# Optimization experiments

Measured on AMD Instinct MI355X. Metric: run time of the kernel, lower is better.

Reference implementation:

```python
import jax, jax.numpy as jnp
import numpy as np

N = 50000
E = 1600000
F_IN = 3
C = 40

def _linear_params(key, fan_in, fan_out):
    k1, k2 = jax.random.split(key)
    bound = 1.0 / np.sqrt(fan_in)
    W = jax.random.uniform(k1, (fan_in, fan_out), jnp.float32, -bound, bound)
    b = jax.random.uniform(k2, (fan_out,), jnp.float32, -bound, bound)
    return W, b

def setup_inputs() -> dict:
    key = jax.random.key(0)
    ks = jax.random.split(key, 9)
    x = jax.random.normal(ks[0], (N, F_IN), jnp.float32)
    pos = jax.random.normal(ks[1], (N, 3), jnp.float32)
    edge_index = jax.random.randint(ks[2], (2, E), 0, N, jnp.int64)
    W1, b1 = _linear_params(ks[3], F_IN + 3, 64)   # local_nn layer 1
    W2, b2 = _linear_params(ks[4], 64, 64)          # local_nn layer 2
    W3, b3 = _linear_params(ks[5], 64, 128)         # global_nn layer 1
    W4, b4 = _linear_params(ks[6], 128, 1024)       # global_nn layer 2
    W5, b5 = _linear_params(ks[7], 1024, 64)        # global_nn layer 3
    Wf, bf = _linear_params(ks[8], 64, C)           # fc
    return {"x": x, "pos": pos, "edge_index": edge_index,
            "W1": W1, "b1": b1, "W2": W2, "b2": b2,
            "W3": W3, "b3": b3, "W4": W4, "b4": b4,
            "W5": W5, "b5": b5, "Wf": Wf, "bf": bf}

def reference(x, pos, edge_index, W1, b1, W2, b2, W3, b3, W4, b4, W5, b5, Wf, bf):
    # PyG PointNetConv: add self-loops by default
    loop = jnp.arange(N, dtype=edge_index.dtype)
    src = jnp.concatenate([edge_index[0], loop])  # j
    dst = jnp.concatenate([edge_index[1], loop])  # i
    # message: local_nn(concat(x_j, pos_j - pos_i))  -> [E+N, 64]
    msg_in = jnp.concatenate([x[src], pos[src] - pos[dst]], axis=1)
    h = jax.nn.relu(msg_in @ W1 + b1)
    h = h @ W2 + b2
    # max-aggregate to destination nodes
    agg = jax.ops.segment_max(h, dst, num_segments=N)
    # global_nn
    g = jax.nn.relu(agg @ W3 + b3)
    g = jax.nn.relu(g @ W4 + b4)
    g = g @ W5 + b5
    # trailing relu + fc + log_softmax
    out = jax.nn.relu(g) @ Wf + bf
    return jax.nn.log_softmax(out, axis=1)
```

## Files before the change

### kernel.cpp

```cpp
#include <hip/hip_runtime.h>
#include <cstddef>
#include <cmath>

typedef __attribute__((ext_vector_type(8))) short bf16x8;
typedef __attribute__((ext_vector_type(4))) float f32x4;

static __device__ __forceinline__ f32x4 mfma16(bf16x8 a, bf16x8 b, f32x4 c) {
    return __builtin_amdgcn_mfma_f32_16x16x32_bf16(a, b, c, 0, 0, 0);
}
static __device__ __forceinline__ unsigned short f2bf(float f) {
    unsigned int u = __float_as_uint(f);
    return (unsigned short)((u + 0x7FFFu + ((u >> 16) & 1u)) >> 16);
}

#define NBK 256

__global__ __launch_bounds__(256) void k_hist(const int* __restrict__ ei, int E,
                                              unsigned int* __restrict__ ghist) {
    __shared__ unsigned int h[NBK];
    int tid = threadIdx.x;
    h[tid] = 0u;
    __syncthreads();
    int idx = blockIdx.x * 256 + tid;
    int e0 = idx * 4;
    if (e0 + 3 < E) {
        int4 d = ((const int4*)(ei + E))[idx];
        atomicAdd(&h[d.x >> 8], 1u);
        atomicAdd(&h[d.y >> 8], 1u);
        atomicAdd(&h[d.z >> 8], 1u);
        atomicAdd(&h[d.w >> 8], 1u);
    } else {
        for (int e = e0; e < E; ++e) atomicAdd(&h[ei[E + e] >> 8], 1u);
    }
    __syncthreads();
    unsigned int c = h[tid];
    if (c) atomicAdd(&ghist[tid], c);
}

__global__ __launch_bounds__(256) void k_bscan(const unsigned int* __restrict__ ghist,
                                               unsigned int* __restrict__ bbase,
                                               unsigned int* __restrict__ gcur) {
    __shared__ unsigned int s[NBK];
    int t = threadIdx.x;
    unsigned int c = ghist[t];
    s[t] = c;
    __syncthreads();
    for (int d = 1; d < 256; d <<= 1) {
        unsigned int v = (t >= d) ? s[t - d] : 0u;
        __syncthreads();
        s[t] += v;
        __syncthreads();
    }
    bbase[t] = s[t] - c;
    gcur[t] = 0u;
}

__global__ __launch_bounds__(256) void k_bin(const int* __restrict__ ei, int E,
                                             const unsigned int* __restrict__ bbase,
                                             unsigned int* __restrict__ gcur,
                                             unsigned int* __restrict__ pairs) {
    __shared__ unsigned int h[NBK];
    __shared__ unsigned int base[NBK];
    int tid = threadIdx.x;
    h[tid] = 0u;
    __syncthreads();
    int idx = blockIdx.x * 256 + tid;
    int e0 = idx * 4;
    unsigned int vals[4]; int bs[4]; unsigned int rk[4]; int cnt4 = 0;
    if (e0 + 3 < E) {
        int4 s = ((const int4*)ei)[idx];
        int4 d = ((const int4*)(ei + E))[idx];
        int sa[4] = {s.x, s.y, s.z, s.w};
        int da[4] = {d.x, d.y, d.z, d.w};
        cnt4 = 4;
#pragma unroll
        for (int j = 0; j < 4; ++j) {
            bs[j] = da[j] >> 8;
            vals[j] = (unsigned int)sa[j] | ((unsigned int)(da[j] & 255) << 16);
            rk[j] = atomicAdd(&h[bs[j]], 1u);
        }
    } else {
        for (int e = e0; e < E; ++e) {
            int j = cnt4++;
            int sv = ei[e], dv = ei[E + e];
            bs[j] = dv >> 8;
            vals[j] = (unsigned int)sv | ((unsigned int)(dv & 255) << 16);
            rk[j] = atomicAdd(&h[bs[j]], 1u);
        }
    }
    __syncthreads();
    unsigned int c = h[tid];
    base[tid] = c ? atomicAdd(&gcur[tid], c) : 0u;
    __syncthreads();
    for (int j = 0; j < cnt4; ++j)
        pairs[bbase[bs[j]] + base[bs[j]] + rk[j]] = vals[j];
}

__global__ __launch_bounds__(256) void k_build(const unsigned int* __restrict__ ghist,
                                               const unsigned int* __restrict__ bbase,
                                               const unsigned int* __restrict__ pairs,
                                               unsigned int* __restrict__ list,
                                               unsigned int* __restrict__ off,
                                               unsigned int* __restrict__ deg, int N) {
    __shared__ unsigned int cntL[NBK];
    __shared__ unsigned int s[NBK];
    __shared__ unsigned int curL[NBK];
    int b = blockIdx.x, t = threadIdx.x;
    unsigned int gstart = bbase[b];
    unsigned int m = ghist[b];
    cntL[t] = 0u;
    __syncthreads();
    for (unsigned int i = t; i < m; i += 256u)
        atomicAdd(&cntL[(pairs[gstart + i] >> 16) & 255u], 1u);
    __syncthreads();
    unsigned int c = cntL[t];
    s[t] = c;
    __syncthreads();
    for (int d = 1; d < 256; d <<= 1) {
        unsigned int v = (t >= d) ? s[t - d] : 0u;
        __syncthreads();
        s[t] += v;
        __syncthreads();
    }
    unsigned int excl = s[t] - c;
    int dst = b * 256 + t;
    if (dst < N) { off[dst] = gstart + excl; deg[dst] = c; }
    curL[t] = excl;
    __syncthreads();
    for (unsigned int i = t; i < m; i += 256u) {
        unsigned int v = pairs[gstart + i];
        unsigned int p = atomicAdd(&curL[(v >> 16) & 255u], 1u);
        list[gstart + p] = v & 0xFFFFu;
    }
}

__global__ void k_convert(const float* __restrict__ W1, const float* __restrict__ W2,
                          const float* __restrict__ W3, const float* __restrict__ W4,
                          const float* __restrict__ W5,
                          unsigned short* __restrict__ W1bt, unsigned short* __restrict__ W2bt,
                          unsigned short* __restrict__ W3bt, unsigned short* __restrict__ W4bt,
                          unsigned short* __restrict__ W5ct) {
    int id = blockIdx.x * 256 + threadIdx.x;
    if (id < 2048) {
        int n = id >> 5, k = id & 31;
        W1bt[id] = (k < 6) ? f2bf(W1[k * 64 + n]) : (unsigned short)0;
    } else if (id < 2048 + 4096) {
        int t = id - 2048;
        int n = t >> 6, k = t & 63;
        W2bt[t] = f2bf(W2[k * 64 + n]);
    } else if (id < 6144 + 8192) {
        int t = id - 6144;
        int n = t >> 6, k = t & 63;
        W3bt[t] = f2bf(W3[k * 128 + n]);
    } else if (id < 14336 + 131072) {
        int t = id - 14336;
        int n = t >> 7, k = t & 127;
        W4bt[t] = f2bf(W4[k * 1024 + n]);
    } else if (id < 145408 + 65536) {
        int t = id - 145408;
        int ch = t >> 11, rem = t & 2047;
        int n = rem >> 5, kl = rem & 31;
        W5ct[t] = f2bf(W5[(ch * 32 + kl) * 64 + n]);
    }
}

#define TPB_E 256
#define EDGE_WPB 4
__global__ __launch_bounds__(TPB_E, 3) void edge_kernel(
    const float* __restrict__ x, const float* __restrict__ pos,
    const unsigned int* __restrict__ off, const unsigned int* __restrict__ deg,
    const unsigned int* __restrict__ list,
    const unsigned short* __restrict__ W1bt, const float* __restrict__ b1,
    const unsigned short* __restrict__ W2bt, const float* __restrict__ b2,
    float* __restrict__ agg, int N, int dstStride)
{
    __shared__ __align__(16) short Hs[4][16 * 72];

    int tid = threadIdx.x;
    int lane = tid & 63;
    int w = tid >> 6;
    int lm = lane & 15;
    int quad = lane >> 4;
    short* H = Hs[w];
    int dst0 = blockIdx.x * EDGE_WPB + w;

    bf16x8 B1f[4], B2f[4][2];
    float b1c[4], b2c[4];
#pragma unroll
    for (int nt = 0; nt < 4; ++nt) {
        B1f[nt] = *(const bf16x8*)&W1bt[(nt * 16 + lm) * 32 + quad * 8];
        B2f[nt][0] = *(const bf16x8*)&W2bt[(nt * 16 + lm) * 64 + quad * 8];
        B2f[nt][1] = *(const bf16x8*)&W2bt[(nt * 16 + lm) * 64 + 32 + quad * 8];
        b1c[nt] = b1[nt * 16 + lm];
        b2c[nt] = b2[nt * 16 + lm];
    }

    for (int dst = dst0; dst < N; dst += dstStride) {
        unsigned int o0 = off[dst];
        int ecnt = (int)deg[dst];
        int M = ecnt + 1;
        float pi0 = pos[dst * 3 + 0], pi1 = pos[dst * 3 + 1], pi2 = pos[dst * 3 + 2];

        float m0 = -INFINITY, m1 = -INFINITY, m2 = -INFINITY, m3 = -INFINITY;

        for (int base = 0; base < M; base += 16) {
            bf16x8 A = {0, 0, 0, 0, 0, 0, 0, 0};
            if (quad == 0) {
                int i = min(base + lm, M - 1);
                int s = (i == 0) ? dst : (int)list[o0 + i - 1];
                A[0] = (short)f2bf(x[s * 3 + 0]);
                A[1] = (short)f2bf(x[s * 3 + 1]);
                A[2] = (short)f2bf(x[s * 3 + 2]);
                A[3] = (short)f2bf(pos[s * 3 + 0] - pi0);
                A[4] = (short)f2bf(pos[s * 3 + 1] - pi1);
                A[5] = (short)f2bf(pos[s * 3 + 2] - pi2);
            }
#pragma unroll
            for (int nt = 0; nt < 4; ++nt) {
                f32x4 c = {0.f, 0.f, 0.f, 0.f};
                c = mfma16(A, B1f[nt], c);
#pragma unroll
                for (int r = 0; r < 4; ++r) {
                    float v = fmaxf(c[r] + b1c[nt], 0.f);
                    H[(quad * 4 + r) * 72 + nt * 16 + lm] = (short)f2bf(v);
                }
            }
            bf16x8 A2a = *(const bf16x8*)&H[lm * 72 + quad * 8];
            bf16x8 A2b = *(const bf16x8*)&H[lm * 72 + 32 + quad * 8];
            {
                f32x4 c = {0.f, 0.f, 0.f, 0.f};
                c = mfma16(A2a, B2f[0][0], c); c = mfma16(A2b, B2f[0][1], c);
                m0 = fmaxf(m0, fmaxf(fmaxf(c[0], c[1]), fmaxf(c[2], c[3])));
            }
            {
                f32x4 c = {0.f, 0.f, 0.f, 0.f};
                c = mfma16(A2a, B2f[1][0], c); c = mfma16(A2b, B2f[1][1], c);
                m1 = fmaxf(m1, fmaxf(fmaxf(c[0], c[1]), fmaxf(c[2], c[3])));
            }
            {
                f32x4 c = {0.f, 0.f, 0.f, 0.f};
                c = mfma16(A2a, B2f[2][0], c); c = mfma16(A2b, B2f[2][1], c);
                m2 = fmaxf(m2, fmaxf(fmaxf(c[0], c[1]), fmaxf(c[2], c[3])));
            }
            {
                f32x4 c = {0.f, 0.f, 0.f, 0.f};
                c = mfma16(A2a, B2f[3][0], c); c = mfma16(A2b, B2f[3][1], c);
                m3 = fmaxf(m3, fmaxf(fmaxf(c[0], c[1]), fmaxf(c[2], c[3])));
            }
        }

        m0 = fmaxf(m0, __shfl_xor(m0, 16, 64)); m0 = fmaxf(m0, __shfl_xor(m0, 32, 64));
        m1 = fmaxf(m1, __shfl_xor(m1, 16, 64)); m1 = fmaxf(m1, __shfl_xor(m1, 32, 64));
        m2 = fmaxf(m2, __shfl_xor(m2, 16, 64)); m2 = fmaxf(m2, __shfl_xor(m2, 32, 64));
        m3 = fmaxf(m3, __shfl_xor(m3, 16, 64)); m3 = fmaxf(m3, __shfl_xor(m3, 32, 64));

        float mv = (quad == 0) ? m0 : (quad == 1) ? m1 : (quad == 2) ? m2 : m3;
        agg[(size_t)dst * 64 + lane] = mv + b2c[quad];
    }
}

#define NNODE 64
__global__ __launch_bounds__(256, 3) void node_kernel(
    const float* __restrict__ agg,
    const unsigned short* __restrict__ W3bt, const float* __restrict__ b3,
    const unsigned short* __restrict__ W4bt, const float* __restrict__ b4,
    const unsigned short* __restrict__ W5ct, const float* __restrict__ b5,
    const float* __restrict__ Wf, const float* __restrict__ bf,
    float* __restrict__ out, int N)
{
    __shared__ __align__(16) char smem[50176];
    short* G1t = (short*)smem;
    float* G3f = (float*)smem;
    short* G2t = (short*)(smem + 17408);
    short* Wb4 = (short*)(smem + 22528);
    short* Wb5 = (short*)(smem + 39936);
    float* os  = (float*)(smem + 17408);

    int tid = threadIdx.x;
    int lane = tid & 63;
    int wm = tid >> 6;
    int lm = lane & 15;
    int quad = lane >> 4;
    int n0 = blockIdx.x * NNODE;

    auto stage = [&](int ch, int buf) {
        const unsigned short* g4 = W4bt + (size_t)ch * 4096;
        short* d4 = Wb4 + buf * 4352;
#pragma unroll
        for (int it = 0; it < 2; ++it) {
            int v = tid + it * 256;
            *(int4*)&d4[(v >> 4) * 136 + (v & 15) * 8] = *(const int4*)(g4 + v * 8);
        }
        const unsigned short* g5 = W5ct + (size_t)ch * 2048;
        short* d5 = Wb5 + buf * 2560;
        {
            int v = tid;
            *(int4*)&d5[(v >> 2) * 40 + (v & 3) * 8] = *(const int4*)(g5 + v * 8);
        }
    };

    stage(0, 0);

    {
        int arow = min(n0 + wm * 16 + lm, N - 1);
        bf16x8 A3[2];
#pragma unroll
        for (int f = 0; f < 2; ++f) {
            const float* p = agg + (size_t)arow * 64 + f * 32 + quad * 8;
            float4 u = *(const float4*)p;
            float4 v = *(const float4*)(p + 4);
            bf16x8 t;
            t[0] = (short)f2bf(u.x); t[1] = (short)f2bf(u.y);
            t[2] = (short)f2bf(u.z); t[3] = (short)f2bf(u.w);
            t[4] = (short)f2bf(v.x); t[5] = (short)f2bf(v.y);
            t[6] = (short)f2bf(v.z); t[7] = (short)f2bf(v.w);
            A3[f] = t;
        }
#pragma unroll
        for (int nt = 0; nt < 8; ++nt) {
            const unsigned short* wb = W3bt + (nt * 16 + lm) * 64 + quad * 8;
            f32x4 c = {0.f, 0.f, 0.f, 0.f};
            c = mfma16(*(const bf16x8*)wb, A3[0], c);
            c = mfma16(*(const bf16x8*)(wb + 32), A3[1], c);
            float4 bb = *(const float4*)&b3[nt * 16 + quad * 4];
            unsigned int u0 = (unsigned int)f2bf(fmaxf(c[0] + bb.x, 0.f)) |
                              ((unsigned int)f2bf(fmaxf(c[1] + bb.y, 0.f)) << 16);
            unsigned int u1 = (unsigned int)f2bf(fmaxf(c[2] + bb.z, 0.f)) |
                              ((unsigned int)f2bf(fmaxf(c[3] + bb.w, 0.f)) << 16);
            *(uint2*)&G1t[(wm * 16 + lm) * 136 + nt * 16 + quad * 4] = make_uint2(u0, u1);
        }
    }

    bf16x8 A4[4];
#pragma unroll
    for (int f = 0; f < 4; ++f)
        A4[f] = *(const bf16x8*)&G1t[(wm * 16 + lm) * 136 + f * 32 + quad * 8];

    f32x4 acc3[4];
#pragma unroll
    for (int nt = 0; nt < 4; ++nt) {
        float b = b5[nt * 16 + lm];
        acc3[nt][0] = b; acc3[nt][1] = b; acc3[nt][2] = b; acc3[nt][3] = b;
    }

    __syncthreads();

    for (int ch = 0; ch < 32; ++ch) {
        int buf = ch & 1;
        if (ch < 31) stage(ch + 1, buf ^ 1);

        const short* w4b = Wb4 + buf * 4352;
        const short* w5b = Wb5 + buf * 2560;

#pragma unroll
        for (int t = 0; t < 2; ++t) {
            f32x4 c = {0.f, 0.f, 0.f, 0.f};
#pragma unroll
            for (int kc = 0; kc < 4; ++kc)
                c = mfma16(*(const bf16x8*)&w4b[(t * 16 + lm) * 136 + kc * 32 + quad * 8],
                           A4[kc], c);
            float4 bb = *(const float4*)&b4[ch * 32 + t * 16 + quad * 4];
            unsigned int u0 = (unsigned int)f2bf(fmaxf(c[0] + bb.x, 0.f)) |
                              ((unsigned int)f2bf(fmaxf(c[1] + bb.y, 0.f)) << 16);
            unsigned int u1 = (unsigned int)f2bf(fmaxf(c[2] + bb.z, 0.f)) |
                              ((unsigned int)f2bf(fmaxf(c[3] + bb.w, 0.f)) << 16);
            *(uint2*)&G2t[(wm * 16 + lm) * 40 + t * 16 + quad * 4] = make_uint2(u0, u1);
        }
        bf16x8 A5 = *(const bf16x8*)&G2t[(wm * 16 + lm) * 40 + quad * 8];
#pragma unroll
        for (int nt = 0; nt < 4; ++nt)
            acc3[nt] = mfma16(A5, *(const bf16x8*)&w5b[(nt * 16 + lm) * 40 + quad * 8],
                              acc3[nt]);
        __syncthreads();
    }

#pragma unroll
    for (int nt = 0; nt < 4; ++nt)
#pragma unroll
        for (int r = 0; r < 4; ++r)
            G3f[(wm * 16 + quad * 4 + r) * 68 + nt * 16 + lm] = fmaxf(acc3[nt][r], 0.f);
    __syncthreads();

    for (int idx = tid; idx < NNODE * 40; idx += 256) {
        int ln = idx / 40;
        int c = idx - ln * 40;
        float o = bf[c];
#pragma unroll 4
        for (int j = 0; j < 64; ++j)
            o = fmaf(G3f[ln * 68 + j], Wf[j * 40 + c], o);
        os[ln * 41 + c] = o;
    }
    __syncthreads();

    if (tid < NNODE && n0 + tid < N) {
        int ln = tid;
        float mx = os[ln * 41 + 0];
#pragma unroll
        for (int c = 1; c < 40; ++c) mx = fmaxf(mx, os[ln * 41 + c]);
        float s = 0.f;
#pragma unroll
        for (int c = 0; c < 40; ++c) s += expf(os[ln * 41 + c] - mx);
        float ls = logf(s) + mx;
        float* op = out + (size_t)(n0 + tid) * 40;
#pragma unroll
        for (int c = 0; c < 40; ++c) op[c] = os[ln * 41 + c] - ls;
    }
}

extern "C" void kernel_launch(void* const* d_in, const int* in_sizes, int n_in,
                              void* d_out, int out_size, void* d_ws, size_t ws_size,
                              hipStream_t stream) {
    const float* x   = (const float*)d_in[0];
    const float* pos = (const float*)d_in[1];
    const int*   ei  = (const int*)d_in[2];
    const float* W1  = (const float*)d_in[3];
    const float* b1  = (const float*)d_in[4];
    const float* W2  = (const float*)d_in[5];
    const float* b2  = (const float*)d_in[6];
    const float* W3  = (const float*)d_in[7];
    const float* b3  = (const float*)d_in[8];
    const float* W4  = (const float*)d_in[9];
    const float* b4  = (const float*)d_in[10];
    const float* W5  = (const float*)d_in[11];
    const float* b5  = (const float*)d_in[12];
    const float* Wf  = (const float*)d_in[13];
    const float* bf  = (const float*)d_in[14];
    float* out = (float*)d_out;

    int Nn = in_sizes[0] / 3;
    int E  = in_sizes[2] / 2;

    char* w = (char*)d_ws;
    size_t p = 0;
    auto take = [&](size_t bytes) { size_t q = p; p = (p + bytes + 255) & ~size_t(255); return (void*)(w + q); };
    unsigned int*   off   = (unsigned int*)take((size_t)Nn * 4);
    unsigned int*   deg   = (unsigned int*)take((size_t)Nn * 4);
    unsigned int*   ghist = (unsigned int*)take(NBK * 4);
    unsigned int*   bbase = (unsigned int*)take(NBK * 4);
    unsigned int*   gcur  = (unsigned int*)take(NBK * 4);
    unsigned int*   list  = (unsigned int*)take((size_t)E * 4);
    float*          agg   = (float*)take((size_t)Nn * 64 * 4);
    unsigned int*   pairs = (unsigned int*)agg;
    unsigned short* W1bt = (unsigned short*)take(2048 * 2);
    unsigned short* W2bt = (unsigned short*)take(4096 * 2);
    unsigned short* W3bt = (unsigned short*)take(8192 * 2);
    unsigned short* W4bt = (unsigned short*)take(131072 * 2);
    unsigned short* W5ct = (unsigned short*)take(65536 * 2);

    k_convert<<<(2048 + 4096 + 8192 + 131072 + 65536 + 255) / 256, 256, 0, stream>>>(
        W1, W2, W3, W4, W5, W1bt, W2bt, W3bt, W4bt, W5ct);

    hipMemsetAsync(ghist, 0, NBK * 4, stream);
    int q4 = (E + 3) / 4;
    int gb = (q4 + 255) / 256;
    k_hist<<<gb, 256, 0, stream>>>(ei, E, ghist);
    k_bscan<<<1, 256, 0, stream>>>(ghist, bbase, gcur);
    k_bin<<<gb, 256, 0, stream>>>(ei, E, bbase, gcur, pairs);
    int nb = (Nn + 255) >> 8;
    k_build<<<nb, 256, 0, stream>>>(ghist, bbase, pairs, list, off, deg, Nn);

    int totalWaves = (Nn + 3) / 4;
    int eBlocks = (totalWaves + EDGE_WPB - 1) / EDGE_WPB;
    int dstStride = eBlocks * EDGE_WPB;
    edge_kernel<<<eBlocks, TPB_E, 0, stream>>>(
        x, pos, off, deg, list, W1bt, b1, W2bt, b2, agg, Nn, dstStride);

    node_kernel<<<(Nn + NNODE - 1) / NNODE, 256, 0, stream>>>(
        agg, W3bt, b3, W4bt, b4, W5ct, b5, Wf, bf, out, Nn);
}
```

Baseline: 357.0 us.

## Read W4/W5 fragments directly from global and process 32 rows per wave

The node kernel drops the LDS double-buffered staging of W4/W5 chunks and their per-chunk block barriers. Each wave now loads weight fragments straight from global/L2 into registers and reuses each one across two 16-row node tiles, with 128 nodes per block. The fc and log_softmax tail becomes per-wave and barrier-free. This trades LDS staging traffic and syncs for more global loads per wave and higher register pressure, which may reduce occupancy.

Measured after the change: 390.6 us. 1.09x slower.

```diff
diff --git a/kernel.cpp b/kernel.cpp
--- a/kernel.cpp
+++ b/kernel.cpp
@@ -139,7 +139,7 @@
                           const float* __restrict__ W5,
                           unsigned short* __restrict__ W1bt, unsigned short* __restrict__ W2bt,
                           unsigned short* __restrict__ W3bt, unsigned short* __restrict__ W4bt,
-                          unsigned short* __restrict__ W5ct) {
+                          unsigned short* __restrict__ W5bt) {
     int id = blockIdx.x * 256 + threadIdx.x;
     if (id < 2048) {
         int n = id >> 5, k = id & 31;
@@ -158,9 +158,8 @@
         W4bt[t] = f2bf(W4[k * 1024 + n]);
     } else if (id < 145408 + 65536) {
         int t = id - 145408;
-        int ch = t >> 11, rem = t & 2047;
-        int n = rem >> 5, kl = rem & 31;
-        W5ct[t] = f2bf(W5[(ch * 32 + kl) * 64 + n]);
+        int n = t >> 10, k = t & 1023;
+        W5bt[t] = f2bf(W5[k * 64 + n]);
     }
 }
 
@@ -259,22 +258,19 @@
     }
 }
 
-#define NNODE 64
+#define NNODE 128
 __global__ __launch_bounds__(256, 3) void node_kernel(
     const float* __restrict__ agg,
     const unsigned short* __restrict__ W3bt, const float* __restrict__ b3,
     const unsigned short* __restrict__ W4bt, const float* __restrict__ b4,
-    const unsigned short* __restrict__ W5ct, const float* __restrict__ b5,
+    const unsigned short* __restrict__ W5bt, const float* __restrict__ b5,
     const float* __restrict__ Wf, const float* __restrict__ bf,
     float* __restrict__ out, int N)
 {
-    __shared__ __align__(16) char smem[50176];
+    __shared__ __align__(16) char smem[45056];
     short* G1t = (short*)smem;
     float* G3f = (float*)smem;
-    short* G2t = (short*)(smem + 17408);
-    short* Wb4 = (short*)(smem + 22528);
-    short* Wb5 = (short*)(smem + 39936);
-    float* os  = (float*)(smem + 17408);
+    short* G2t = (short*)(smem + 34816);
 
     int tid = threadIdx.x;
     int lane = tid & 63;
@@ -282,27 +278,11 @@
     int lm = lane & 15;
     int quad = lane >> 4;
     int n0 = blockIdx.x * NNODE;
-
-    auto stage = [&](int ch, int buf) {
-        const unsigned short* g4 = W4bt + (size_t)ch * 4096;
-        short* d4 = Wb4 + buf * 4352;
-#pragma unroll
-        for (int it = 0; it < 2; ++it) {
-            int v = tid + it * 256;
-            *(int4*)&d4[(v >> 4) * 136 + (v & 15) * 8] = *(const int4*)(g4 + v * 8);
-        }
-        const unsigned short* g5 = W5ct + (size_t)ch * 2048;
-        short* d5 = Wb5 + buf * 2560;
-        {
-            int v = tid;
-            *(int4*)&d5[(v >> 2) * 40 + (v & 3) * 8] = *(const int4*)(g5 + v * 8);
-        }
-    };
-
-    stage(0, 0);
-
-    {
-        int arow = min(n0 + wm * 16 + lm, N - 1);
+    int wbase = wm * 32;
+
+#pragma unroll
+    for (int rf = 0; rf < 2; ++rf) {
+        int arow = min(n0 + wbase + rf * 16 + lm, N - 1);
         bf16x8 A3[2];
 #pragma unroll
         for (int f = 0; f < 2; ++f) {
@@ -327,83 +307,95 @@
                               ((unsigned int)f2bf(fmaxf(c[1] + bb.y, 0.f)) << 16);
             unsigned int u1 = (unsigned int)f2bf(fmaxf(c[2] + bb.z, 0.f)) |
                               ((unsigned int)f2bf(fmaxf(c[3] + bb.w, 0.f)) << 16);
-            *(uint2*)&G1t[(wm * 16 + lm) * 136 + nt * 16 + quad * 4] = make_uint2(u0, u1);
-        }
-    }
-
-    bf16x8 A4[4];
-#pragma unroll
-    for (int f = 0; f < 4; ++f)
-        A4[f] = *(const bf16x8*)&G1t[(wm * 16 + lm) * 136 + f * 32 + quad * 8];
-
-    f32x4 acc3[4];
-#pragma unroll
-    for (int nt = 0; nt < 4; ++nt) {
-        float b = b5[nt * 16 + lm];
-        acc3[nt][0] = b; acc3[nt][1] = b; acc3[nt][2] = b; acc3[nt][3] = b;
-    }
-
-    __syncthreads();
+            *(uint2*)&G1t[(wbase + rf * 16 + lm) * 136 + nt * 16 + quad * 4] = make_uint2(u0, u1);
+        }
+    }
+
+    bf16x8 A4[2][4];
+#pragma unroll
+    for (int rf = 0; rf < 2; ++rf)
+#pragma unroll
+        for (int f = 0; f < 4; ++f)
+            A4[rf][f] = *(const bf16x8*)&G1t[(wbase + rf * 16 + lm) * 136 + f * 32 + quad * 8];
+
+    f32x4 acc3[2][4];
+#pragma unroll
+    for (int rf = 0; rf < 2; ++rf)
+#pragma unroll
+        for (int nt = 0; nt < 4; ++nt) {
+            float b = b5[nt * 16 + lm];
+            acc3[rf][nt][0] = b; acc3[rf][nt][1] = b;
+            acc3[rf][nt][2] = b; acc3[rf][nt][3] = b;
+        }
 
     for (int ch = 0; ch < 32; ++ch) {
-        int buf = ch & 1;
-        if (ch < 31) stage(ch + 1, buf ^ 1);
-
-        const short* w4b = Wb4 + buf * 4352;
-        const short* w5b = Wb5 + buf * 2560;
-
 #pragma unroll
         for (int t = 0; t < 2; ++t) {
-            f32x4 c = {0.f, 0.f, 0.f, 0.f};
-#pragma unroll
-            for (int kc = 0; kc < 4; ++kc)
-                c = mfma16(*(const bf16x8*)&w4b[(t * 16 + lm) * 136 + kc * 32 + quad * 8],
-                           A4[kc], c);
+            const unsigned short* w4g = W4bt + (size_t)(ch * 32 + t * 16 + lm) * 128 + quad * 8;
+            bf16x8 w40 = *(const bf16x8*)(w4g);
+            bf16x8 w41 = *(const bf16x8*)(w4g + 32);
+            bf16x8 w42 = *(const bf16x8*)(w4g + 64);
+            bf16x8 w43 = *(const bf16x8*)(w4g + 96);
             float4 bb = *(const float4*)&b4[ch * 32 + t * 16 + quad * 4];
-            unsigned int u0 = (unsigned int)f2bf(fmaxf(c[0] + bb.x, 0.f)) |
-                              ((unsigned int)f2bf(fmaxf(c[1] + bb.y, 0.f)) << 16);
-            unsigned int u1 = (unsigned int)f2bf(fmaxf(c[2] + bb.z, 0.f)) |
-                              ((unsigned int)f2bf(fmaxf(c[3] + bb.w, 0.f)) << 16);
-            *(uint2*)&G2t[(wm * 16 + lm) * 40 + t * 16 + quad * 4] = make_uint2(u0, u1);
-        }
-        bf16x8 A5 = *(const bf16x8*)&G2t[(wm * 16 + lm) * 40 + quad * 8];
+#pragma unroll
+            for (int rf = 0; rf < 2; ++rf) {
+                f32x4 c = {0.f, 0.f, 0.f, 0.f};
+                c = mfma16(w40, A4[rf][0], c);
+                c = mfma16(w41, A4[rf][1], c);
+                c = mfma16(w42, A4[rf][2], c);
+                c = mfma16(w43, A4[rf][3], c);
+                unsigned int u0 = (unsigned int)f2bf(fmaxf(c[0] + bb.x, 0.f)) |
+                                  ((unsigned int)f2bf(fmaxf(c[1] + bb.y, 0.f)) << 16);
+                unsigned int u1 = (unsigned int)f2bf(fmaxf(c[2] + bb.z, 0.f)) |
+                                  ((unsigned int)f2bf(fmaxf(c[3] + bb.w, 0.f)) << 16);
+                *(uint2*)&G2t[(wbase + rf * 16 + lm) * 40 + t * 16 + quad * 4] = make_uint2(u0, u1);
+            }
+        }
+        bf16x8 A5_0 = *(const bf16x8*)&G2t[(wbase + lm) * 40 + quad * 8];
+        bf16x8 A5_1 = *(const bf16x8*)&G2t[(wbase + 16 + lm) * 40 + quad * 8];
+#pragma unroll
+        for (int nt = 0; nt < 4; ++nt) {
+            bf16x8 w5f = *(const bf16x8*)&W5bt[(size_t)(nt * 16 + lm) * 1024 + ch * 32 + quad * 8];
+            acc3[0][nt] = mfma16(A5_0, w5f, acc3[0][nt]);
+            acc3[1][nt] = mfma16(A5_1, w5f, acc3[1][nt]);
+        }
+    }
+
+#pragma unroll
+    for (int rf = 0; rf < 2; ++rf)
 #pragma unroll
         for (int nt = 0; nt < 4; ++nt)
-            acc3[nt] = mfma16(A5, *(const bf16x8*)&w5b[(nt * 16 + lm) * 40 + quad * 8],
-                              acc3[nt]);
-        __syncthreads();
-    }
-
-#pragma unroll
-    for (int nt = 0; nt < 4; ++nt)
-#pragma unroll
-        for (int r = 0; r < 4; ++r)
-            G3f[(wm * 16 + quad * 4 + r) * 68 + nt * 16 + lm] = fmaxf(acc3[nt][r], 0.f);
-    __syncthreads();
-
-    for (int idx = tid; idx < NNODE * 40; idx += 256) {
-        int ln = idx / 40;
-        int c = idx - ln * 40;
-        float o = bf[c];
+#pragma unroll
+            for (int r = 0; r < 4; ++r)
+                G3f[(wbase + rf * 16 + quad * 4 + r) * 68 + nt * 16 + lm] =
+                    fmaxf(acc3[rf][nt][r], 0.f);
+
+    float* osw = (float*)(G2t + (size_t)wbase * 40);
+#pragma unroll
+    for (int half = 0; half < 2; ++half) {
+        for (int i = lane; i < 16 * 40; i += 64) {
+            int ln = i / 40;
+            int c = i - ln * 40;
+            float o = bf[c];
+            const float* g = &G3f[(wbase + half * 16 + ln) * 68];
 #pragma unroll 4
-        for (int j = 0; j < 64; ++j)
-            o = fmaf(G3f[ln * 68 + j], Wf[j * 40 + c], o);
-        os[ln * 41 + c] = o;
-    }
-    __syncthreads();
-
-    if (tid < NNODE && n0 + tid < N) {
-        int ln = tid;
-        float mx = os[ln * 41 + 0];
-#pragma unroll
-        for (int c = 1; c < 40; ++c) mx = fmaxf(mx, os[ln * 41 + c]);
-        float s = 0.f;
-#pragma unroll
-        for (int c = 0; c < 40; ++c) s += expf(os[ln * 41 + c] - mx);
-        float ls = logf(s) + mx;
-        float* op = out + (size_t)(n0 + tid) * 40;
-#pragma unroll
-        for (int c = 0; c < 40; ++c) op[c] = os[ln * 41 + c] - ls;
+            for (int j = 0; j < 64; ++j)
+                o = fmaf(g[j], Wf[j * 40 + c], o);
+            osw[ln * 40 + c] = o;
+        }
+        int node = n0 + wbase + half * 16 + lane;
+        if (lane < 16 && node < N) {
+            float mx = osw[lane * 40 + 0];
+#pragma unroll
+            for (int c = 1; c < 40; ++c) mx = fmaxf(mx, osw[lane * 40 + c]);
+            float s = 0.f;
+#pragma unroll
+            for (int c = 0; c < 40; ++c) s += expf(osw[lane * 40 + c] - mx);
+            float ls = logf(s) + mx;
+            float* op = out + (size_t)node * 40;
+#pragma unroll
+            for (int c = 0; c < 40; ++c) op[c] = osw[lane * 40 + c] - ls;
+        }
     }
 }
 
@@ -445,10 +437,10 @@
     unsigned short* W2bt = (unsigned short*)take(4096 * 2);
     unsigned short* W3bt = (unsigned short*)take(8192 * 2);
     unsigned short* W4bt = (unsigned short*)take(131072 * 2);
-    unsigned short* W5ct = (unsigned short*)take(65536 * 2);
+    unsigned short* W5bt = (unsigned short*)take(65536 * 2);
 
     k_convert<<<(2048 + 4096 + 8192 + 131072 + 65536 + 255) / 256, 256, 0, stream>>>(
-        W1, W2, W3, W4, W5, W1bt, W2bt, W3bt, W4bt, W5ct);
+        W1, W2, W3, W4, W5, W1bt, W2bt, W3bt, W4bt, W5bt);
 
     hipMemsetAsync(ghist, 0, NBK * 4, stream);
     int q4 = (E + 3) / 4;
@@ -466,5 +458,5 @@
         x, pos, off, deg, list, W1bt, b1, W2bt, b2, agg, Nn, dstStride);
 
     node_kernel<<<(Nn + NNODE - 1) / NNODE, 256, 0, stream>>>(
-        agg, W3bt, b3, W4bt, b4, W5ct, b5, Wf, bf, out, Nn);
-}
+        agg, W3bt, b3, W4bt, b4, W5bt, b5, Wf, bf, out, Nn);
+}
```
